# Optimization experiments

Hardware: AMD Instinct MI355X
Metric: run time of the kernel (lower is better)

Reference implementation:

```python
import jax, jax.numpy as jnp
import numpy as np

B = 32          # batch size
N = 32          # image dim -> P = N*N points per sample
P = N * N
F = 64          # point feature dim (= MLP output)
K = 32          # max_neighbors
R = 0.1         # ball-query radius
EPS = 1e-5      # batchnorm eps


def setup_inputs() -> dict:
    key = jax.random.key(0)
    ks = jax.random.split(key, 4)
    NP = B * P
    x = jax.random.normal(ks[0], (NP, F), jnp.float32)
    pos = jax.random.uniform(ks[1], (NP, 2), jnp.float32)
    # module requires exactly N*N points per sample, sorted by batch
    batch = jnp.repeat(jnp.arange(B, dtype=jnp.int32), P)
    # MLP([66,128,64]) params: Linear->BN->ReLU->Linear
    W1 = jax.random.normal(ks[2], (F + 2, 128), jnp.float32) * (1.0 / np.sqrt(F + 2))
    b1 = jnp.zeros((128,), jnp.float32)
    gamma1 = jnp.ones((128,), jnp.float32)
    beta1 = jnp.zeros((128,), jnp.float32)
    W2 = jax.random.normal(ks[3], (128, F), jnp.float32) * (1.0 / np.sqrt(128))
    b2 = jnp.zeros((F,), jnp.float32)
    return {"x": x, "pos": pos, "batch": batch, "W1": W1, "b1": b1,
            "gamma1": gamma1, "beta1": beta1, "W2": W2, "b2": b2}


def reference(x, pos, batch, W1, b1, gamma1, beta1, W2, b2):
    NP = x.shape[0]
    posb = pos.reshape(B, P, 2)
    # pixel (target) index of every query point: batch*N*N + row*N + col
    rows = jnp.clip((pos[:, 1] * N).astype(jnp.int32), 0, N - 1)
    cols = jnp.clip((pos[:, 0] * N).astype(jnp.int32), 0, N - 1)
    pix = batch.astype(jnp.int32) * (N * N) + rows * N + cols          # [NP]
    # radius ball query within each batch sample (deterministic: nearest-K within R)
    d2 = jnp.sum((posb[:, :, None, :] - posb[:, None, :, :]) ** 2, -1)  # [B,P,P]
    d2 = jnp.where(d2 <= R * R, d2, jnp.inf)
    negd, nbr = jax.lax.top_k(-d2, K)                                   # [B,P,K]
    valid = jnp.isfinite(negd)
    src = (jnp.arange(B, dtype=jnp.int32)[:, None, None] * P + nbr).reshape(-1)  # [B*P*K]
    dst = jnp.broadcast_to(pix.reshape(B, P)[:, :, None], (B, P, K)).reshape(-1)
    mask = valid.reshape(-1) & (src != dst)          # remove_self_loops
    # PointNetConv message: concat(x_j, pos_j - pos_i); pos_i indexed by mapped target
    relpos = pos[src] - pos[dst]
    msg_nb = jnp.concatenate([x[src], relpos], -1)                    # [B*P*K, F+2]
    # add_self_loops: edge (i, i) for every node -> relpos = 0
    msg_self = jnp.concatenate([x, jnp.zeros_like(pos)], -1)          # [NP, F+2]
    msg = jnp.concatenate([msg_nb, msg_self], 0)
    m = jnp.concatenate([mask, jnp.ones((NP,), bool)], 0)
    tgt = jnp.concatenate([dst, jnp.arange(NP, dtype=jnp.int32)], 0)
    # MLP: Linear -> BatchNorm(training stats over valid messages) -> ReLU -> Linear
    z = msg @ W1 + b1
    mf = m.astype(z.dtype)[:, None]
    cnt = jnp.sum(mf)
    mean = jnp.sum(z * mf, 0, keepdims=True) / cnt
    var = jnp.sum(((z - mean) ** 2) * mf, 0, keepdims=True) / cnt
    h = jax.nn.relu((z - mean) / jnp.sqrt(var + EPS) * gamma1 + beta1)
    o = h @ W2 + b2                                                    # [M, F]
    # scatter-max aggregation into B*N*N pixel nodes (self loops make all nonempty)
    o = jnp.where(m[:, None], o, -jnp.inf)
    pixel_features = jax.ops.segment_max(o, tgt, num_segments=NP)
    images = pixel_features.reshape(B, N, N, F).transpose(0, 3, 1, 2)
    return images
```

## Files before the change

kernel.cpp:

```cpp
#include <hip/hip_runtime.h>
#include <hip/hip_bf16.h>
#include <hip/hip_fp16.h>
#include <math.h>


#define NPTS   32768
#define KNB    32
#define BN_EPS 1e-5f

#define WS_NBRS     0u
#define WS_NBRCNT   4194304u
#define WS_W2B32    4325376u
#define WS_SCSH     4719616u
#define WS_W2B      4720640u
#define WS_PART     4737024u
#define WS_Y        5265408u
#define WS_SCRATCH  5265408u
#define WS_WB       13654016u
#define WS_QCNT     22042624u
#define WS_QSTART   22173696u
#define WS_QLIST    22304768u
#define WS_ISLOT    22435840u
#define WS_SELF     22566912u
#define WS_SHP      30955520u
#define WS_BQPART   22566912u

typedef __attribute__((ext_vector_type(8))) _Float16 half8;
typedef __attribute__((ext_vector_type(2))) _Float16 half2v;
typedef __attribute__((ext_vector_type(4))) float floatx4;
typedef __attribute__((ext_vector_type(16))) float floatx16;

__device__ __forceinline__ unsigned short f2h_bits(float f) {
    _Float16 h = (_Float16)f;
    return *reinterpret_cast<unsigned short*>(&h);
}
__device__ __forceinline__ float bf_lo(unsigned int w) { return __uint_as_float(w << 16); }
__device__ __forceinline__ float bf_hi(unsigned int w) { return __uint_as_float(w & 0xffff0000u); }
__device__ __forceinline__ unsigned int pack_bf2(float lo, float hi) {
    __hip_bfloat162 hh = __float22bfloat162_rn(make_float2(lo, hi));
    return *reinterpret_cast<unsigned int*>(&hh);
}
__device__ __forceinline__ unsigned int pack_h2(float lo, float hi) {
    half2v hh = { (_Float16)lo, (_Float16)hi };
    return *reinterpret_cast<unsigned int*>(&hh);
}

union ShBQ {
    struct {
        float2 poss[1024];
        float accd[1024], accx[1024], accy[1024];
        unsigned long long cand[4][256];
    } bq;
    struct {
        int cntS[1024], preS[1024], offS[1024], pixOf[1024];
        int wtot[4];
    } pm;
};

__launch_bounds__(256)
__global__ void k_bq(const float* __restrict__ pos,
                     int* __restrict__ nbrs, int* __restrict__ nbr_cnt,
                     float* __restrict__ bqpart,
                     const float* __restrict__ W2, unsigned short* __restrict__ w2b,
                     unsigned short* __restrict__ w2b32,
                     int* __restrict__ qcnt, int* __restrict__ qstart,
                     int* __restrict__ qlist, int* __restrict__ islot) {
    __shared__ ShBQ sh;
    int tid = threadIdx.x;

    if (blockIdx.x < 32) {
        int s = blockIdx.x;
        int gt = s * 256 + tid;
        {
            int j  = gt & 7;
            int L  = (gt >> 3) & 63;
            int ks = (gt >> 9) & 3;
            int t4 = gt >> 11;
            int k = ks * 32 + (L >> 4) * 8 + j;
            int n = t4 * 16 + (L & 15);
            w2b[gt] = f2h_bits(W2[k * 64 + n]);
        }
        {
            int j  = gt & 7;
            int L  = (gt >> 3) & 63;
            int p  = gt >> 9;
            int ks = p >> 1, nh = p & 1;
            int k = ks * 16 + (L >> 5) * 8 + j;
            int n = nh * 32 + (L & 31);
            w2b32[gt] = f2h_bits(W2[k * 64 + n]);
        }
        int base = s << 10;
        for (int i = tid; i < 1024; i += 256) sh.pm.cntS[i] = 0;
        __syncthreads();
        for (int ql = tid; ql < 1024; ql += 256) {
            float2 p = *(const float2*)&pos[2 * (base + ql)];
            int row = min(max((int)(p.y * 32.0f), 0), 31);
            int col = min(max((int)(p.x * 32.0f), 0), 31);
            int pixl = row * 32 + col;
            sh.pm.pixOf[ql] = pixl;
            atomicAdd(&sh.pm.cntS[pixl], 1);
        }
        __syncthreads();
        int a0 = sh.pm.cntS[4 * tid], a1 = sh.pm.cntS[4 * tid + 1];
        int a2 = sh.pm.cntS[4 * tid + 2], a3 = sh.pm.cntS[4 * tid + 3];
        int tsum = a0 + a1 + a2 + a3;
        int lane = tid & 63, wv = tid >> 6;
        int v = tsum;
        for (int o = 1; o < 64; o <<= 1) { int u = __shfl_up(v, o); if (lane >= o) v += u; }
        if (lane == 63) sh.pm.wtot[wv] = v;
        __syncthreads();
        int wbase = 0;
        for (int w = 0; w < wv; ++w) wbase += sh.pm.wtot[w];
        int excl = wbase + v - tsum;
        sh.pm.preS[4 * tid] = excl;
        sh.pm.preS[4 * tid + 1] = excl + a0;
        sh.pm.preS[4 * tid + 2] = excl + a0 + a1;
        sh.pm.preS[4 * tid + 3] = excl + a0 + a1 + a2;
        __syncthreads();
        for (int i = tid; i < 1024; i += 256) sh.pm.offS[i] = sh.pm.preS[i];
        __syncthreads();
        for (int ql = tid; ql < 1024; ql += 256) {
            int p = sh.pm.pixOf[ql];
            int slot = atomicAdd(&sh.pm.offS[p], 1);
            qlist[base + slot] = base + ql;
            islot[base + ql] = base + slot;
        }
        for (int i = tid; i < 1024; i += 256) {
            qcnt[base + i] = sh.pm.cntS[i];
            qstart[base + i] = base + sh.pm.preS[i];
        }
        return;
    }

    int bqphys = blockIdx.x - 32;
    int bqid = (bqphys & 7) * 128 + (bqphys >> 3);
    int wave = tid >> 6, lane = tid & 63;
    int s = bqid >> 5;
    int chunk = bqid & 31;
    int base = s << 10;
    for (int i = tid; i < 1024; i += 256) sh.bq.poss[i] = *(const float2*)&pos[2 * (base + i)];
    for (int i = tid; i < 1024; i += 256) { sh.bq.accd[i] = 0.0f; sh.bq.accx[i] = 0.0f; sh.bq.accy[i] = 0.0f; }
    __syncthreads();
    float2 pr[16];
#pragma unroll
    for (int k = 0; k < 16; ++k) pr[k] = sh.bq.poss[k * 64 + lane];
    unsigned long long lb = (1ull << lane) - 1ull;

    float aD = 0, aE = 0, aF = 0;
    for (int qi = 0; qi < 8; ++qi) {
        int ql = chunk * 32 + wave * 8 + qi;
        int q = base + ql;
        float2 qp = sh.bq.poss[ql];
        int row = min(max((int)(qp.y * 32.0f), 0), 31);
        int col = min(max((int)(qp.x * 32.0f), 0), 31);
        int pixl = row * 32 + col;
        float2 tp = sh.bq.poss[pixl];
        int cnt = 0;
        __builtin_amdgcn_wave_barrier();
#pragma unroll
        for (int k = 0; k < 16; ++k) {
            float dx = pr[k].x - qp.x, dy = pr[k].y - qp.y;
            float d2 = __fadd_rn(__fmul_rn(dx, dx), __fmul_rn(dy, dy));
            bool pred = (d2 <= 0.01f);
            unsigned long long mask = __ballot(pred);
            if (pred) {
                int slot = cnt + (int)__popcll(mask & lb);
                if (slot < 256)
                    sh.bq.cand[wave][slot] = ((unsigned long long)__float_as_uint(d2) << 32)
                                             | (unsigned int)(k * 64 + lane);
            }
            cnt += (int)__popcll(mask);
        }
        cnt = min(cnt, 256);
        __builtin_amdgcn_wave_barrier();
        int osel = 0;
        for (int cb = 0; cb < cnt; cb += 64) {
            int i = cb + lane;
            bool sel = false;
            int j = 0;
            if (i < cnt) {
                unsigned long long key = sh.bq.cand[wave][i];
                j = (int)(key & 0xffffffffu);
                if (cnt <= KNB) {
                    sel = (j != pixl);
                } else {
                    int rank = 0;
                    for (int t = 0; t < cnt; ++t) rank += (sh.bq.cand[wave][t] < key) ? 1 : 0;
                    sel = (rank < KNB) && (j != pixl);
                }
            }
            unsigned long long mask = __ballot(sel);
            if (sel) {
                int slot = osel + (int)__popcll(mask & lb);
                nbrs[q * KNB + slot] = base + j;
                float rx = sh.bq.poss[j].x - tp.x, ry = sh.bq.poss[j].y - tp.y;
                aD += rx * rx; aE += rx * ry; aF += ry * ry;
                atomicAdd(&sh.bq.accd[j], 1.0f);
                atomicAdd(&sh.bq.accx[j], tp.x);
                atomicAdd(&sh.bq.accy[j], tp.y);
            }
            osel += (int)__popcll(mask);
        }
        if (lane >= osel && lane < KNB) nbrs[q * KNB + lane] = base;
        if (lane == 0) nbr_cnt[q] = osel;
    }
#pragma unroll
    for (int o = 1; o < 64; o <<= 1) {
        aD += __shfl_xor(aD, o); aE += __shfl_xor(aE, o); aF += __shfl_xor(aF, o);
    }
    __syncthreads();
    float* pb = &bqpart[bqid * 3076];
    for (int i = tid; i < 1024; i += 256) {
        pb[i] = sh.bq.accd[i]; pb[1024 + i] = sh.bq.accx[i]; pb[2048 + i] = sh.bq.accy[i];
    }
    if (tid == 0) { pb[3072] = aD; pb[3073] = aE; pb[3074] = aF; }
}

__launch_bounds__(512)
__global__ void k_y(const float* __restrict__ x, const float* __restrict__ W1,
                    const float* __restrict__ b1, const float* __restrict__ pos,
                    const float* __restrict__ bqpart,
                    unsigned int* __restrict__ yb, float* __restrict__ partials) {
    __shared__ float w1s[64 * 128];
    __shared__ float stage[8][512];
    __shared__ float lsum[515];
    __shared__ float degS[128], stxS[128], styS[128];
    int tid = threadIdx.x;
    int vb = (blockIdx.x & 7) * 32 + (blockIdx.x >> 3);
    int nblock = vb * 128;
    for (int i = tid; i < 64 * 128; i += 512) w1s[i] = W1[i];
    for (int i = tid; i < 515; i += 512) lsum[i] = 0.0f;
    if (tid < 128) {
        int n = nblock + tid;
        int s = n >> 10, off = n & 1023;
        const float* pb = &bqpart[(s * 32) * 3076];
        float d = 0, xx = 0, yy = 0;
        for (int j = 0; j < 32; ++j) {
            d  += pb[j * 3076 + off];
            xx += pb[j * 3076 + 1024 + off];
            yy += pb[j * 3076 + 2048 + off];
        }
        degS[tid] = d; stxS[tid] = xx; styS[tid] = yy;
    }
    __syncthreads();
    int wave = tid >> 6, lane = tid & 63;
    int f0 = 2 * lane, f1 = 2 * lane + 1;
    float b10 = b1[f0], b11 = b1[f1];
    float* st = &stage[wave][0];
    float P0 = 0, Q0 = 0, R0 = 0, S0 = 0, P1 = 0, Q1 = 0, R1 = 0, S1 = 0;
    float sB = 0, sC = 0, sDeg = 0;

    for (int it = 0; it < 2; ++it) {
        int nbase = nblock + (wave * 2 + it) * 8;
        __builtin_amdgcn_wave_barrier();
#pragma unroll
        for (int mm = 0; mm < 8; ++mm)
            st[mm * 64 + lane] = x[(nbase + mm) * 64 + lane];
        __builtin_amdgcn_wave_barrier();
        float z0[8], z1[8];
#pragma unroll
        for (int mm = 0; mm < 8; ++mm) { z0[mm] = b10; z1[mm] = b11; }
        for (int k4 = 0; k4 < 16; ++k4) {
            float2 wv0 = *(const float2*)&w1s[(k4 * 4 + 0) * 128 + f0];
            float2 wv1 = *(const float2*)&w1s[(k4 * 4 + 1) * 128 + f0];
            float2 wv2 = *(const float2*)&w1s[(k4 * 4 + 2) * 128 + f0];
            float2 wv3 = *(const float2*)&w1s[(k4 * 4 + 3) * 128 + f0];
#pragma unroll
            for (int mm = 0; mm < 8; ++mm) {
                float4 mk = *(const float4*)&st[mm * 64 + k4 * 4];
                z0[mm] += mk.x * wv0.x + mk.y * wv1.x + mk.z * wv2.x + mk.w * wv3.x;
                z1[mm] += mk.x * wv0.y + mk.y * wv1.y + mk.z * wv2.y + mk.w * wv3.y;
            }
        }
#pragma unroll
        for (int mm = 0; mm < 8; ++mm) {
            int n = nbase + mm;
            int li = n - nblock;
            float dg = degS[li];
            float wgt = 1.0f + dg;
            float Bn = dg * pos[2 * n]     - stxS[li];
            float Cn = dg * pos[2 * n + 1] - styS[li];
            float a = z0[mm], bq = z1[mm];
            P0 += wgt * a;  Q0 += wgt * a * a;  R0 += a * Bn;  S0 += a * Cn;
            P1 += wgt * bq; Q1 += wgt * bq * bq; R1 += bq * Bn; S1 += bq * Cn;
            sB += Bn; sC += Cn; sDeg += dg;
            yb[n * 64 + lane] = pack_bf2(a, bq);
        }
        __builtin_amdgcn_wave_barrier();
    }
    atomicAdd(&lsum[f0], P0);        atomicAdd(&lsum[f1], P1);
    atomicAdd(&lsum[128 + f0], Q0);  atomicAdd(&lsum[128 + f1], Q1);
    atomicAdd(&lsum[256 + f0], R0);  atomicAdd(&lsum[256 + f1], R1);
    atomicAdd(&lsum[384 + f0], S0);  atomicAdd(&lsum[384 + f1], S1);
    if (lane == 0) {
        atomicAdd(&lsum[512], sB);
        atomicAdd(&lsum[513], sC);
        atomicAdd(&lsum[514], sDeg);
    }
    __syncthreads();
    for (int i = tid; i < 515; i += 512) partials[blockIdx.x * 516 + i] = lsum[i];
}

__global__ void k_finalize(const float* __restrict__ gamma, const float* __restrict__ beta,
                           const float* __restrict__ W1, const float* __restrict__ partials,
                           const float* __restrict__ bqpart, float* __restrict__ scsh) {
    __shared__ float red[515];
    __shared__ float sDEF[3];
    int tid = threadIdx.x;
    if (tid < 3) sDEF[tid] = 0.0f;
    for (int i = tid; i < 515; i += 256) {
        float s = 0;
        for (int b = 0; b < 256; ++b) s += partials[b * 516 + i];
        red[i] = s;
    }
    __syncthreads();
    {
        float td = 0, te = 0, tf = 0;
        for (int b = tid; b < 1024; b += 256) {
            const float* pb = &bqpart[b * 3076 + 3072];
            td += pb[0]; te += pb[1]; tf += pb[2];
        }
        atomicAdd(&sDEF[0], td); atomicAdd(&sDEF[1], te); atomicAdd(&sDEF[2], tf);
    }
    __syncthreads();
    if (tid < 128) {
        int f = tid;
        float P = red[f], Q = red[128 + f], R = red[256 + f], S = red[384 + f];
        float SB = red[512], SC = red[513], SDeg = red[514];
        float u = W1[8192 + f], v = W1[8320 + f];
        float cntv = 32768.0f + SDeg;
        float mean = (P + u * SB + v * SC) / cntv;
        float E2 = (Q + 2.0f * u * R + 2.0f * v * S
                    + u * u * sDEF[0] + 2.0f * u * v * sDEF[1] + v * v * sDEF[2]) / cntv;
        float var = E2 - mean * mean;
        float sc = gamma[f] / sqrtf(var + BN_EPS);
        scsh[f] = sc;
        scsh[128 + f] = beta[f] - mean * sc;
    }
}

__launch_bounds__(256)
__global__ void k_self(const unsigned int* __restrict__ yb, const float* __restrict__ pos,
                       const float* __restrict__ W1, const float* __restrict__ scsh,
                       const unsigned short* __restrict__ w2b, const float* __restrict__ b2,
                       const int* __restrict__ qcnt,
                       unsigned int* __restrict__ wbuf, unsigned int* __restrict__ shpbuf,
                       float* __restrict__ selfbuf, float* __restrict__ out) {
    __shared__ unsigned short hbuf[4][16 * 136];
    int tid = threadIdx.x, wave = tid >> 6, lane = tid & 63;
    unsigned short* hb = hbuf[wave];
    half8 bfrag[4][4];
#pragma unroll
    for (int t = 0; t < 4; ++t)
#pragma unroll
        for (int ks = 0; ks < 4; ++ks)
            bfrag[t][ks] = *(const half8*)&w2b[((t * 4 + ks) * 64 + lane) * 8];
    int f0 = 2 * lane;
    float sc0 = scsh[f0],     sh0 = scsh[128 + f0];
    float sc1 = scsh[f0 + 1], sh1 = scsh[129 + f0];
    float u0 = W1[8192 + f0], v0 = W1[8320 + f0];
    float u1 = W1[8193 + f0], v1 = W1[8321 + f0];
    float b2v0 = b2[(lane & 15)],      b2v1 = b2[16 + (lane & 15)];
    float b2v2 = b2[32 + (lane & 15)], b2v3 = b2[48 + (lane & 15)];

    int vb = (blockIdx.x & 7) * 64 + (blockIdx.x >> 3);
    int nbase = (vb * 4 + wave) * 16;
#pragma unroll
    for (int c = 0; c < 2; ++c) {
        unsigned int yw[8];
#pragma unroll
        for (int j = 0; j < 8; ++j)
            yw[j] = yb[(nbase + c * 8 + j) * 64 + lane];
#pragma unroll
        for (int j = 0; j < 8; ++j) {
            int e = c * 8 + j;
            int nn = nbase + e;
            float y0 = bf_lo(yw[j]), y1 = bf_hi(yw[j]);
            float h0 = fmaxf(y0 * sc0 + sh0, 0.0f);
            float h1 = fmaxf(y1 * sc1 + sh1, 0.0f);
            *(unsigned int*)&hb[e * 136 + f0] = pack_h2(h0, h1);
            float px = pos[2 * nn], py = pos[2 * nn + 1];
            float ts0 = (px * u0 + py * v0) * sc0;
            float ts1 = (px * u1 + py * v1) * sc1;
            wbuf[nn * 64 + lane]   = pack_h2(y0 * sc0 + ts0, y1 * sc1 + ts1);
            shpbuf[nn * 64 + lane] = pack_h2(sh0 - ts0, sh1 - ts1);
        }
    }
    __builtin_amdgcn_wave_barrier();
    floatx4 acc0 = {0,0,0,0}, acc1 = {0,0,0,0}, acc2 = {0,0,0,0}, acc3 = {0,0,0,0};
#pragma unroll
    for (int ks = 0; ks < 4; ++ks) {
        half8 a = *(const half8*)&hb[(lane & 15) * 136 + ks * 32 + (lane >> 4) * 8];
        acc0 = __builtin_amdgcn_mfma_f32_16x16x32_f16(a, bfrag[0][ks], acc0, 0, 0, 0);
        acc1 = __builtin_amdgcn_mfma_f32_16x16x32_f16(a, bfrag[1][ks], acc1, 0, 0, 0);
        acc2 = __builtin_amdgcn_mfma_f32_16x16x32_f16(a, bfrag[2][ks], acc2, 0, 0, 0);
        acc3 = __builtin_amdgcn_mfma_f32_16x16x32_f16(a, bfrag[3][ks], acc3, 0, 0, 0);
    }
    int nrow = nbase + (lane >> 4) * 4;
#pragma unroll
    for (int r = 0; r < 4; ++r) {
        int n = nrow + r;
        float o0 = acc0[r] + b2v0, o1 = acc1[r] + b2v1;
        float o2 = acc2[r] + b2v2, o3 = acc3[r] + b2v3;
        selfbuf[n * 64 + (lane & 15)]      = o0;
        selfbuf[n * 64 + 16 + (lane & 15)] = o1;
        selfbuf[n * 64 + 32 + (lane & 15)] = o2;
        selfbuf[n * 64 + 48 + (lane & 15)] = o3;
        if (qcnt[n] == 0) {
            int obase = (n >> 10) * 65536 + (n & 1023);
            out[obase + ((lane & 15)) * 1024]      = o0;
            out[obase + (16 + (lane & 15)) * 1024] = o1;
            out[obase + (32 + (lane & 15)) * 1024] = o2;
            out[obase + (48 + (lane & 15)) * 1024] = o3;
        }
    }
}

__launch_bounds__(256, 2)
__global__ void k_out(const unsigned int* __restrict__ wbuf,
                      const unsigned int* __restrict__ shpbuf,
                      const float* __restrict__ pos,
                      const unsigned short* __restrict__ w2b32, const float* __restrict__ b2,
                      const int* __restrict__ nbrs, const int* __restrict__ nbr_cnt,
                      const int* __restrict__ islot, float* __restrict__ scratch) {
    int tid = threadIdx.x, wave = tid >> 6, lane = tid & 63;
    half8 bfrag[8][2];
#pragma unroll
    for (int ks = 0; ks < 8; ++ks)
#pragma unroll
        for (int nh = 0; nh < 2; ++nh)
            bfrag[ks][nh] = *(const half8*)&w2b32[((ks * 2 + nh) * 64 + lane) * 8];
    float b2l = b2[lane];
    int kc = (lane >> 5) * 4;
    int vb = (blockIdx.x & 7) * 256 + (blockIdx.x >> 3);
    int wid = vb * 4 + wave;
    int qb = wid * 4;

    int4 mv  = *(const int4*)&nbr_cnt[qb];
    int4 isv = *(const int4*)&islot[qb];
    int nv0 = nbrs[(qb + 0) * KNB + (lane & 31)];
    int nv1 = nbrs[(qb + 1) * KNB + (lane & 31)];
    int nv2 = nbrs[(qb + 2) * KNB + (lane & 31)];
    int nv3 = nbrs[(qb + 3) * KNB + (lane & 31)];
    float4 pA = *(const float4*)&pos[2 * qb];
    float4 pB = *(const float4*)&pos[2 * qb + 4];
    int sbase = (qb >> 10) << 10;
    int pixq0 = sbase + min(max((int)(pA.y * 32.0f), 0), 31) * 32 + min(max((int)(pA.x * 32.0f), 0), 31);
    int pixq1 = sbase + min(max((int)(pA.w * 32.0f), 0), 31) * 32 + min(max((int)(pA.z * 32.0f), 0), 31);
    int pixq2 = sbase + min(max((int)(pB.y * 32.0f), 0), 31) * 32 + min(max((int)(pB.x * 32.0f), 0), 31);
    int pixq3 = sbase + min(max((int)(pB.w * 32.0f), 0), 31) * 32 + min(max((int)(pB.z * 32.0f), 0), 31);

    uint4 gA[8], gB[8], sv[8];
    floatx16 acc0, acc1;

#define ISSUE_G(dst, nv) do {                                               \
        const unsigned int* wp_ = &wbuf[(nv) * 64 + kc];                    \
        _Pragma("unroll")                                                   \
        for (int ks_ = 0; ks_ < 8; ++ks_) dst[ks_] = *(const uint4*)&wp_[ks_ * 8]; \
    } while (0)

#define LOAD_SV(pixq) do {                                                  \
        const unsigned int* sp_ = &shpbuf[(pixq) * 64 + kc];                \
        _Pragma("unroll")                                                   \
        for (int ks_ = 0; ks_ < 8; ++ks_) sv[ks_] = *(const uint4*)&sp_[ks_ * 8]; \
    } while (0)

#define DO_MFMA(g) do {                                                     \
        acc0 = (floatx16){}; acc1 = (floatx16){};                           \
        __builtin_amdgcn_s_setprio(1);                                      \
        _Pragma("unroll")                                                   \
        for (int ks_ = 0; ks_ < 8; ++ks_) {                                 \
            union { unsigned int u[4]; half8 h8; } af_;                     \
            uint4 gg_ = g[ks_], ss_ = sv[ks_];                              \
            _Pragma("unroll")                                               \
            for (int qd_ = 0; qd_ < 4; ++qd_) {                             \
                unsigned int wd_ = (qd_ == 0) ? gg_.x : (qd_ == 1) ? gg_.y  \
                                 : (qd_ == 2) ? gg_.z : gg_.w;              \
                unsigned int sd_ = (qd_ == 0) ? ss_.x : (qd_ == 1) ? ss_.y  \
                                 : (qd_ == 2) ? ss_.z : ss_.w;              \
                half2v wh_ = *reinterpret_cast<half2v*>(&wd_);              \
                half2v sh_ = *reinterpret_cast<half2v*>(&sd_);              \
                half2v zz_ = { (_Float16)0.0f, (_Float16)0.0f };            \
                half2v hh_ = __builtin_elementwise_max(wh_ + sh_, zz_);     \
                af_.u[qd_] = *reinterpret_cast<unsigned int*>(&hh_);        \
            }                                                               \
            acc0 = __builtin_amdgcn_mfma_f32_32x32x16_f16(af_.h8, bfrag[ks_][0], acc0, 0, 0, 0); \
            acc1 = __builtin_amdgcn_mfma_f32_32x32x16_f16(af_.h8, bfrag[ks_][1], acc1, 0, 0, 0); \
        }                                                                   \
        __builtin_amdgcn_s_setprio(0);                                      \
    } while (0)

#define EPILOG(m, isq) do {                                                 \
        int rbase_ = 4 * (lane >> 5);                                       \
        float v0_ = -INFINITY, v1_ = -INFINITY;                             \
        _Pragma("unroll")                                                   \
        for (int i_ = 0; i_ < 16; ++i_) {                                   \
            int r_ = (i_ & 3) + 8 * (i_ >> 2) + rbase_;                     \
            bool ok_ = r_ < (m);                                            \
            v0_ = fmaxf(v0_, ok_ ? acc0[i_] : -INFINITY);                   \
            v1_ = fmaxf(v1_, ok_ ? acc1[i_] : -INFINITY);                   \
        }                                                                   \
        v0_ = fmaxf(v0_, __shfl_xor(v0_, 32));                              \
        v1_ = fmaxf(v1_, __shfl_xor(v1_, 32));                              \
        float vf_ = ((lane < 32) ? v0_ : v1_) + b2l;                        \
        scratch[(isq) * 64 + lane] = vf_;                                   \
    } while (0)

    ISSUE_G(gA, nv0);
    ISSUE_G(gB, nv1);
    LOAD_SV(pixq0); DO_MFMA(gA); EPILOG(mv.x, isv.x);
    ISSUE_G(gA, nv2);
    LOAD_SV(pixq1); DO_MFMA(gB); EPILOG(mv.y, isv.y);
    ISSUE_G(gB, nv3);
    LOAD_SV(pixq2); DO_MFMA(gA); EPILOG(mv.z, isv.z);
    LOAD_SV(pixq3); DO_MFMA(gB); EPILOG(mv.w, isv.w);

#undef ISSUE_G
#undef LOAD_SV
#undef DO_MFMA
#undef EPILOG
}

__launch_bounds__(256)
__global__ void k_gather(const float* __restrict__ scratch, const float* __restrict__ selfbuf,
                         const int* __restrict__ qcnt, const int* __restrict__ qstart,
                         float* __restrict__ out) {
    int tid = threadIdx.x, wave = tid >> 6, lane = tid & 63;
    int vb = (blockIdx.x & 7) * 1024 + (blockIdx.x >> 3);
    int n = vb * 4 + wave;
    int c = qcnt[n];
    if (c == 0) return;
    int qs = qstart[n];
    float v = selfbuf[n * 64 + lane];
    for (int i = 0; i < c; ++i)
        v = fmaxf(v, scratch[(qs + i) * 64 + lane]);
    out[(n >> 10) * 65536 + lane * 1024 + (n & 1023)] = v;
}

extern "C" void kernel_launch(void* const* d_in, const int* in_sizes, int n_in,
                              void* d_out, int out_size, void* d_ws, size_t ws_size,
                              hipStream_t stream) {
    const float* x     = (const float*)d_in[0];
    const float* pos   = (const float*)d_in[1];
    const float* W1    = (const float*)d_in[3];
    const float* b1    = (const float*)d_in[4];
    const float* gamma = (const float*)d_in[5];
    const float* beta  = (const float*)d_in[6];
    const float* W2    = (const float*)d_in[7];
    const float* b2    = (const float*)d_in[8];
    float* out = (float*)d_out;
    char* ws = (char*)d_ws;
    int*   nbrs     = (int*)(ws + WS_NBRS);
    int*   nbr_cnt  = (int*)(ws + WS_NBRCNT);
    float* scsh     = (float*)(ws + WS_SCSH);
    unsigned short* w2b = (unsigned short*)(ws + WS_W2B);
    unsigned short* w2b32 = (unsigned short*)(ws + WS_W2B32);
    float* partials = (float*)(ws + WS_PART);
    unsigned int* yb = (unsigned int*)(ws + WS_Y);
    float* scratch  = (float*)(ws + WS_SCRATCH);
    unsigned int* wbuf = (unsigned int*)(ws + WS_WB);
    int* qcnt   = (int*)(ws + WS_QCNT);
    int* qstart = (int*)(ws + WS_QSTART);
    int* qlist  = (int*)(ws + WS_QLIST);
    int* islot  = (int*)(ws + WS_ISLOT);
    float* selfbuf = (float*)(ws + WS_SELF);
    unsigned int* shpbuf = (unsigned int*)(ws + WS_SHP);
    float* bqpart   = (float*)(ws + WS_BQPART);

    k_bq<<<1056, 256, 0, stream>>>(pos, nbrs, nbr_cnt, bqpart, W2, w2b, w2b32,
                                   qcnt, qstart, qlist, islot);
    k_y<<<256, 512, 0, stream>>>(x, W1, b1, pos, bqpart, yb, partials);
    k_finalize<<<1, 256, 0, stream>>>(gamma, beta, W1, partials, bqpart, scsh);
    k_self<<<NPTS / 64, 256, 0, stream>>>(yb, pos, W1, scsh, w2b, b2, qcnt,
                                          wbuf, shpbuf, selfbuf, out);
    k_out<<<NPTS / 16, 256, 0, stream>>>(wbuf, shpbuf, pos, w2b32, b2,
                                         nbrs, nbr_cnt, islot, scratch);
    k_gather<<<NPTS / 4, 256, 0, stream>>>(scratch, selfbuf, qcnt, qstart, out);
}
```

Measured before the change: 238.9 us.

## Fuse BN finalize and gather into producers via last-block atomic counters

Drops the single-block finalize kernel and the separate gather kernel. The last k_y block to finish, detected with an atomic counter and threadfences, now reduces the partials and writes the BN scale and shift. In k_out, each wave bumps a per-pixel completion counter, and whichever wave is last for a pixel runs the scatter-max gather and writes the output. This removes two kernel launches and their inter-kernel gaps, at the cost of extra atomics, fences, and a serial tail in the last k_y block.

Result: slower. 659.0 us (+175.9%).

```diff
diff --git a/kernel.cpp b/kernel.cpp
--- a/kernel.cpp
+++ b/kernel.cpp
@@ -11,6 +11,8 @@
 #define WS_NBRS     0u
 #define WS_NBRCNT   4194304u
 #define WS_W2B32    4325376u
+#define WS_KCNT     4341760u
+#define WS_PIXDONE  4345856u
 #define WS_SCSH     4719616u
 #define WS_W2B      4720640u
 #define WS_PART     4737024u
@@ -64,12 +66,14 @@
                      const float* __restrict__ W2, unsigned short* __restrict__ w2b,
                      unsigned short* __restrict__ w2b32,
                      int* __restrict__ qcnt, int* __restrict__ qstart,
-                     int* __restrict__ qlist, int* __restrict__ islot) {
+                     int* __restrict__ qlist, int* __restrict__ islot,
+                     int* __restrict__ kcnt, int* __restrict__ pixdone) {
     __shared__ ShBQ sh;
     int tid = threadIdx.x;
 
     if (blockIdx.x < 32) {
         int s = blockIdx.x;
+        if (s == 0 && tid == 0) kcnt[0] = 0;
         int gt = s * 256 + tid;
         {
             int j  = gt & 7;
@@ -128,6 +132,7 @@
         for (int i = tid; i < 1024; i += 256) {
             qcnt[base + i] = sh.pm.cntS[i];
             qstart[base + i] = base + sh.pm.preS[i];
+            pixdone[base + i] = 0;
         }
         return;
     }
@@ -220,11 +225,15 @@
 __global__ void k_y(const float* __restrict__ x, const float* __restrict__ W1,
                     const float* __restrict__ b1, const float* __restrict__ pos,
                     const float* __restrict__ bqpart,
-                    unsigned int* __restrict__ yb, float* __restrict__ partials) {
+                    unsigned int* __restrict__ yb, float* __restrict__ partials,
+                    const float* __restrict__ gamma, const float* __restrict__ beta,
+                    float* __restrict__ scsh, int* __restrict__ kcnt) {
     __shared__ float w1s[64 * 128];
     __shared__ float stage[8][512];
     __shared__ float lsum[515];
     __shared__ float degS[128], stxS[128], styS[128];
+    __shared__ int finflag;
+    __shared__ float sDEF[3];
     int tid = threadIdx.x;
     int vb = (blockIdx.x & 7) * 32 + (blockIdx.x >> 3);
     int nblock = vb * 128;
@@ -299,43 +308,45 @@
     }
     __syncthreads();
     for (int i = tid; i < 515; i += 512) partials[blockIdx.x * 516 + i] = lsum[i];
-}
-
-__global__ void k_finalize(const float* __restrict__ gamma, const float* __restrict__ beta,
-                           const float* __restrict__ W1, const float* __restrict__ partials,
-                           const float* __restrict__ bqpart, float* __restrict__ scsh) {
-    __shared__ float red[515];
-    __shared__ float sDEF[3];
-    int tid = threadIdx.x;
-    if (tid < 3) sDEF[tid] = 0.0f;
-    for (int i = tid; i < 515; i += 256) {
-        float s = 0;
-        for (int b = 0; b < 256; ++b) s += partials[b * 516 + i];
-        red[i] = s;
-    }
+
     __syncthreads();
-    {
-        float td = 0, te = 0, tf = 0;
-        for (int b = tid; b < 1024; b += 256) {
-            const float* pb = &bqpart[b * 3076 + 3072];
-            td += pb[0]; te += pb[1]; tf += pb[2];
-        }
-        atomicAdd(&sDEF[0], td); atomicAdd(&sDEF[1], te); atomicAdd(&sDEF[2], tf);
+    if (tid == 0) {
+        __threadfence();
+        finflag = (atomicAdd(kcnt, 1) == 255) ? 1 : 0;
     }
     __syncthreads();
-    if (tid < 128) {
-        int f = tid;
-        float P = red[f], Q = red[128 + f], R = red[256 + f], S = red[384 + f];
-        float SB = red[512], SC = red[513], SDeg = red[514];
-        float u = W1[8192 + f], v = W1[8320 + f];
-        float cntv = 32768.0f + SDeg;
-        float mean = (P + u * SB + v * SC) / cntv;
-        float E2 = (Q + 2.0f * u * R + 2.0f * v * S
-                    + u * u * sDEF[0] + 2.0f * u * v * sDEF[1] + v * v * sDEF[2]) / cntv;
-        float var = E2 - mean * mean;
-        float sc = gamma[f] / sqrtf(var + BN_EPS);
-        scsh[f] = sc;
-        scsh[128 + f] = beta[f] - mean * sc;
+    if (finflag) {
+        __threadfence();
+        if (tid < 3) sDEF[tid] = 0.0f;
+        for (int i = tid; i < 515; i += 512) {
+            float ssum = 0;
+            for (int b = 0; b < 256; ++b) ssum += partials[b * 516 + i];
+            lsum[i] = ssum;
+        }
+        __syncthreads();
+        {
+            float td = 0, te = 0, tf = 0;
+            for (int b = tid; b < 1024; b += 512) {
+                const float* pbb = &bqpart[b * 3076 + 3072];
+                td += pbb[0]; te += pbb[1]; tf += pbb[2];
+            }
+            atomicAdd(&sDEF[0], td); atomicAdd(&sDEF[1], te); atomicAdd(&sDEF[2], tf);
+        }
+        __syncthreads();
+        if (tid < 128) {
+            int f = tid;
+            float P = lsum[f], Q = lsum[128 + f], R = lsum[256 + f], S = lsum[384 + f];
+            float SB = lsum[512], SC = lsum[513], SDeg = lsum[514];
+            float u = W1[8192 + f], v2 = W1[8320 + f];
+            float cntv = 32768.0f + SDeg;
+            float mean = (P + u * SB + v2 * SC) / cntv;
+            float E2 = (Q + 2.0f * u * R + 2.0f * v2 * S
+                        + u * u * sDEF[0] + 2.0f * u * v2 * sDEF[1] + v2 * v2 * sDEF[2]) / cntv;
+            float var = E2 - mean * mean;
+            float sc = gamma[f] / sqrtf(var + BN_EPS);
+            scsh[f] = sc;
+            scsh[128 + f] = beta[f] - mean * sc;
+        }
     }
 }
 
@@ -422,7 +433,10 @@
                       const float* __restrict__ pos,
                       const unsigned short* __restrict__ w2b32, const float* __restrict__ b2,
                       const int* __restrict__ nbrs, const int* __restrict__ nbr_cnt,
-                      const int* __restrict__ islot, float* __restrict__ scratch) {
+                      const int* __restrict__ islot,
+                      const int* __restrict__ qcnt, const int* __restrict__ qstart,
+                      const float* __restrict__ selfbuf, int* __restrict__ pixdone,
+                      float* __restrict__ scratch, float* __restrict__ out) {
     int tid = threadIdx.x, wave = tid >> 6, lane = tid & 63;
     half8 bfrag[8][2];
 #pragma unroll
@@ -506,6 +520,14 @@
         scratch[(isq) * 64 + lane] = vf_;                                   \
     } while (0)
 
+#define GATHER(p) do {                                                      \
+        int qs_ = qstart[(p)], c2_ = qcnt[(p)];                             \
+        float v_ = selfbuf[(p) * 64 + lane];                                \
+        for (int i_ = 0; i_ < c2_; ++i_)                                    \
+            v_ = fmaxf(v_, scratch[(qs_ + i_) * 64 + lane]);                \
+        out[((p) >> 10) * 65536 + lane * 1024 + ((p) & 1023)] = v_;         \
+    } while (0)
+
     ISSUE_G(gA, nv0);
     ISSUE_G(gB, nv1);
     LOAD_SV(pixq0); DO_MFMA(gA); EPILOG(mv.x, isv.x);
@@ -515,26 +537,28 @@
     LOAD_SV(pixq2); DO_MFMA(gA); EPILOG(mv.z, isv.z);
     LOAD_SV(pixq3); DO_MFMA(gB); EPILOG(mv.w, isv.w);
 
+    __threadfence();
+    int wonmask = 0;
+    if (lane == 0) {
+        if (atomicAdd(&pixdone[pixq0], 1) == qcnt[pixq0] - 1) wonmask |= 1;
+        if (atomicAdd(&pixdone[pixq1], 1) == qcnt[pixq1] - 1) wonmask |= 2;
+        if (atomicAdd(&pixdone[pixq2], 1) == qcnt[pixq2] - 1) wonmask |= 4;
+        if (atomicAdd(&pixdone[pixq3], 1) == qcnt[pixq3] - 1) wonmask |= 8;
+    }
+    wonmask = __shfl(wonmask, 0);
+    if (wonmask) {
+        __threadfence();
+        if (wonmask & 1) GATHER(pixq0);
+        if (wonmask & 2) GATHER(pixq1);
+        if (wonmask & 4) GATHER(pixq2);
+        if (wonmask & 8) GATHER(pixq3);
+    }
+
 #undef ISSUE_G
 #undef LOAD_SV
 #undef DO_MFMA
 #undef EPILOG
-}
-
-__launch_bounds__(256)
-__global__ void k_gather(const float* __restrict__ scratch, const float* __restrict__ selfbuf,
-                         const int* __restrict__ qcnt, const int* __restrict__ qstart,
-                         float* __restrict__ out) {
-    int tid = threadIdx.x, wave = tid >> 6, lane = tid & 63;
-    int vb = (blockIdx.x & 7) * 1024 + (blockIdx.x >> 3);
-    int n = vb * 4 + wave;
-    int c = qcnt[n];
-    if (c == 0) return;
-    int qs = qstart[n];
-    float v = selfbuf[n * 64 + lane];
-    for (int i = 0; i < c; ++i)
-        v = fmaxf(v, scratch[(qs + i) * 64 + lane]);
-    out[(n >> 10) * 65536 + lane * 1024 + (n & 1023)] = v;
+#undef GATHER
 }
 
 extern "C" void kernel_launch(void* const* d_in, const int* in_sizes, int n_in,
@@ -566,14 +590,17 @@
     float* selfbuf = (float*)(ws + WS_SELF);
     unsigned int* shpbuf = (unsigned int*)(ws + WS_SHP);
     float* bqpart   = (float*)(ws + WS_BQPART);
+    int* kcnt    = (int*)(ws + WS_KCNT);
+    int* pixdone = (int*)(ws + WS_PIXDONE);
 
     k_bq<<<1056, 256, 0, stream>>>(pos, nbrs, nbr_cnt, bqpart, W2, w2b, w2b32,
-                                   qcnt, qstart, qlist, islot);
-    k_y<<<256, 512, 0, stream>>>(x, W1, b1, pos, bqpart, yb, partials);
-    k_finalize<<<1, 256, 0, stream>>>(gamma, beta, W1, partials, bqpart, scsh);
+                                   qcnt, qstart, qlist, islot, kcnt, pixdone);
+    k_y<<<256, 512, 0, stream>>>(x, W1, b1, pos, bqpart, yb, partials,
+                                 gamma, beta, scsh, kcnt);
     k_self<<<NPTS / 64, 256, 0, stream>>>(yb, pos, W1, scsh, w2b, b2, qcnt,
                                           wbuf, shpbuf, selfbuf, out);
     k_out<<<NPTS / 16, 256, 0, stream>>>(wbuf, shpbuf, pos, w2b32, b2,
-                                         nbrs, nbr_cnt, islot, scratch);
-    k_gather<<<NPTS / 4, 256, 0, stream>>>(scratch, selfbuf, qcnt, qstart, out);
-}
+                                         nbrs, nbr_cnt, islot,
+                                         qcnt, qstart, selfbuf, pixdone,
+                                         scratch, out);
+}
```
